# Kernel optimization log

Measured on AMD Instinct MI355X. Metric: run time of the kernel, lower is better.

The kernel has to match this reference:

```python
import jax, jax.numpy as jnp
import numpy as np

L = 4            # num_layers
N_GENES = 2048   # col_dim: rows of x, PPI graph nodes
N_CELLS = 2048   # row_dim: cols of x, KNN graph nodes
E_KNN = 30720    # ~k=15 per cell
E_PPI = 65536    # ~avg degree 32 per gene
NEG_SLOPE = 0.01 # nn.LeakyReLU default


def setup_inputs() -> dict:
    key = jax.random.key(0)
    ks = jax.random.split(key, 9)
    x = jax.random.normal(ks[0], (N_GENES, N_CELLS), jnp.float32)
    knn_edge_index = jax.random.randint(ks[1], (2, E_KNN), 0, N_CELLS)
    ppi_edge_index = jax.random.randint(ks[2], (2, E_PPI), 0, N_GENES)
    s_c = 1.0 / np.sqrt(N_GENES)  # cols side feature dim = col_dim
    s_r = 1.0 / np.sqrt(N_CELLS)  # rows side feature dim = row_dim
    col_Wl = jax.random.normal(ks[3], (L, N_GENES, N_GENES), jnp.float32) * s_c
    col_bl = jnp.zeros((L, N_GENES), jnp.float32)
    col_Wr = jax.random.normal(ks[4], (L, N_GENES, N_GENES), jnp.float32) * s_c
    row_Wl = jax.random.normal(ks[5], (L, N_CELLS, N_CELLS), jnp.float32) * s_r
    row_bl = jnp.zeros((L, N_CELLS), jnp.float32)
    row_Wr = jax.random.normal(ks[6], (L, N_CELLS, N_CELLS), jnp.float32) * s_r
    return dict(x=x, knn_edge_index=knn_edge_index, ppi_edge_index=ppi_edge_index,
                col_Wl=col_Wl, col_bl=col_bl, col_Wr=col_Wr,
                row_Wl=row_Wl, row_bl=row_bl, row_Wr=row_Wr)


def _sage(h, edge_index, Wl, bl, Wr):
    # PyG SAGEConv (mean aggr): out = lin_l(mean_{j->i} h_j) + lin_r(h_i)
    src, tgt = edge_index[0], edge_index[1]
    n = h.shape[0]
    summed = jax.ops.segment_sum(h[src], tgt, num_segments=n)          # [n, d]
    cnt = jax.ops.segment_sum(jnp.ones((src.shape[0],), h.dtype), tgt, num_segments=n)
    mean = summed / jnp.maximum(cnt, 1.0)[:, None]
    return mean @ Wl + bl + h @ Wr


def reference(x, knn_edge_index, ppi_edge_index,
              col_Wl, col_bl, col_Wr, row_Wl, row_bl, row_Wr):
    # Dropout is identity in eval mode; layer = SAGEConv -> LeakyReLU on both sides.
    h = x  # [N_GENES, N_CELLS]
    for i in range(L):
        # cols side: operate on h.T [N_CELLS, N_GENES] over KNN graph
        h = jax.nn.leaky_relu(_sage(h.T, knn_edge_index, col_Wl[i], col_bl[i], col_Wr[i]),
                              negative_slope=NEG_SLOPE).T
        # rows side: operate on h [N_GENES, N_CELLS] over PPI graph
        h = jax.nn.leaky_relu(_sage(h, ppi_edge_index, row_Wl[i], row_bl[i], row_Wr[i]),
                              negative_slope=NEG_SLOPE)
    return h
```

## Files before the change

kernel.cpp:

```cpp
#include <hip/hip_runtime.h>
#include <stdint.h>

#define NSZ 2048
#define NLAYERS 4

typedef __attribute__((ext_vector_type(4))) float f32x4;
typedef __attribute__((ext_vector_type(4))) _Float16 f16x4;
typedef __attribute__((ext_vector_type(8))) _Float16 f16x8;

__device__ __forceinline__ void gload_lds16(const void* g, void* l) {
  __builtin_amdgcn_global_load_lds((const __attribute__((address_space(1))) void*)g,
                                   (__attribute__((address_space(3))) void*)l, 16, 0, 0);
}

__global__ void k_zero(int* __restrict__ p, int n) {
  int i = blockIdx.x * 256 + threadIdx.x;
  if (i < n) p[i] = 0;
}

__global__ void k_count(const int* __restrict__ tgt, int E, int* __restrict__ cnt) {
  int e = blockIdx.x * 256 + threadIdx.x;
  if (e < E) atomicAdd(&cnt[tgt[e] & (NSZ - 1)], 1);
}

__global__ __launch_bounds__(1024) void k_scan(
    const int* __restrict__ cntA, int* __restrict__ offA, int* __restrict__ curA,
    float* __restrict__ invA, int EA,
    const int* __restrict__ cntB, int* __restrict__ offB, int* __restrict__ curB,
    float* __restrict__ invB, int EB) {
  const int* cnt; int* off; int* cur; float* inv; int E;
  if (blockIdx.x == 0) { cnt = cntA; off = offA; cur = curA; inv = invA; E = EA; }
  else                 { cnt = cntB; off = offB; cur = curB; inv = invB; E = EB; }
  __shared__ int sa[2048], sb[2048];
  int t = threadIdx.x;
  sa[t] = cnt[t]; sa[t + 1024] = cnt[t + 1024];
  __syncthreads();
  int* s = sa; int* d = sb;
  for (int dd = 1; dd < 2048; dd <<= 1) {
    for (int i = t; i < 2048; i += 1024)
      d[i] = s[i] + ((i >= dd) ? s[i - dd] : 0);
    __syncthreads();
    int* tmp = s; s = d; d = tmp;
  }
  for (int i = t; i < 2048; i += 1024) {
    int o = (i == 0) ? 0 : s[i - 1];
    off[i] = o; cur[i] = o;
    int c = cnt[i];
    inv[i] = 1.0f / (float)((c > 1) ? c : 1);
  }
  if (t == 0) off[2048] = E;
}

__global__ void k_fill(const int* __restrict__ src, const int* __restrict__ tgt, int E,
                       int* __restrict__ cur, int* __restrict__ srcs) {
  int e = blockIdx.x * 256 + threadIdx.x;
  if (e < E) {
    int p = atomicAdd(&cur[tgt[e] & (NSZ - 1)], 1);
    if (p >= 0 && p < E) srcs[p] = src[e] & (NSZ - 1);
  }
}

__global__ __launch_bounds__(256) void k_transpose_cvt(const float* __restrict__ s,
                                                       _Float16* __restrict__ Ah,
                                                       _Float16* __restrict__ Al) {
  __shared__ float tile[64][65];
  const int tid = threadIdx.x;
  const int r0 = blockIdx.y << 6, c0 = blockIdx.x << 6;
#pragma unroll
  for (int it = 0; it < 4; ++it) {
    int e = it * 256 + tid;
    int r = e >> 4;
    int c = (e & 15) << 2;
    f32x4 v = *(const f32x4*)&s[(size_t)(r0 + r) * NSZ + c0 + c];
#pragma unroll
    for (int j = 0; j < 4; ++j) tile[r][c + j] = v[j];
  }
  __syncthreads();
#pragma unroll
  for (int it = 0; it < 4; ++it) {
    int e = it * 256 + tid;
    int r = e >> 4;
    int c4 = (e & 15) << 2;
    f16x4 hi, lo;
#pragma unroll
    for (int j = 0; j < 4; ++j) {
      float x = tile[c4 + j][r];
      _Float16 h = (_Float16)x;
      hi[j] = h;
      lo[j] = (_Float16)(x - (float)h);
    }
    int m = c0 + r;
    size_t rowb = (size_t)m << 12;
    int byte = ((r0 + c4) << 1) ^ (((m >> 1) & 3) << 4);
    *(f16x4*)((char*)Ah + rowb + byte) = hi;
    *(f16x4*)((char*)Al + rowb + byte) = lo;
  }
}

__global__ __launch_bounds__(256) void k_cvtB(const float* __restrict__ Wl,
                                              const float* __restrict__ Wr,
                                              _Float16* __restrict__ Bh,
                                              _Float16* __restrict__ Bl) {
  __shared__ float tile[64][65];
  const float* W = blockIdx.z ? Wr : Wl;
  const int nbase = blockIdx.z ? NSZ : 0;
  const int tid = threadIdx.x;
  const int k0 = blockIdx.y << 6;
  const int n0 = blockIdx.x << 6;
#pragma unroll
  for (int it = 0; it < 4; ++it) {
    int e = it * 256 + tid;
    int r = e >> 4;
    int c = (e & 15) << 2;
    f32x4 v = *(const f32x4*)&W[(size_t)(k0 + r) * NSZ + n0 + c];
#pragma unroll
    for (int j = 0; j < 4; ++j) tile[r][c + j] = v[j];
  }
  __syncthreads();
#pragma unroll
  for (int it = 0; it < 4; ++it) {
    int e = it * 256 + tid;
    int r = e >> 4;
    int c4 = (e & 15) << 2;
    f16x4 hi, lo;
#pragma unroll
    for (int j = 0; j < 4; ++j) {
      float x = tile[c4 + j][r];
      _Float16 h = (_Float16)x;
      hi[j] = h;
      lo[j] = (_Float16)(x - (float)h);
    }
    int n = nbase + n0 + r;
    size_t rowb = (size_t)n << 12;
    int byte = ((k0 + c4) << 1) ^ (((n >> 1) & 3) << 4);
    *(f16x4*)((char*)Bh + rowb + byte) = hi;
    *(f16x4*)((char*)Bl + rowb + byte) = lo;
  }
}

__global__ __launch_bounds__(256, 2) void k_gemm16(
    const _Float16* __restrict__ Ah, const _Float16* __restrict__ Al,
    const _Float16* __restrict__ Bh, const _Float16* __restrict__ Bl,
    float* __restrict__ C) {
  __shared__ __align__(128) _Float16 lds[2][4][128][32];
  const int tid = threadIdx.x;
  const int w = tid >> 6;
  const int lane = tid & 63;
  int bid = blockIdx.x;
  bid = ((bid & 7) << 6) | (bid >> 3);
  const int bm = bid & 15;
  const int bn = bid >> 4;
  const int m0 = bm << 7;
  const int n0 = bn << 7;
  const int wm = (w & 1) << 6;
  const int wn = (w >> 1) << 6;

  f32x4 acc[4][4];
#pragma unroll
  for (int i = 0; i < 4; ++i)
#pragma unroll
    for (int j = 0; j < 4; ++j)
#pragma unroll
      for (int r = 0; r < 4; ++r) acc[i][j][r] = 0.f;

  const int srow0 = (w << 5) + (lane >> 2);
  const int scol = (lane & 3) << 3;
  const int l15 = lane & 15;
  const int ks16 = (lane >> 4) << 4;

  const size_t aoff = (size_t)(m0 + srow0) * NSZ + scol;
  const size_t boff = (size_t)(n0 + srow0) * NSZ + scol;

#define STAGE(buf, kk)                                                     \
  do {                                                                     \
    _Pragma("unroll") for (int q = 0; q < 2; ++q) {                        \
      const size_t go = (size_t)(q << 4) * NSZ + (kk);                     \
      const int dr = ((w << 1) + q) << 4;                                  \
      gload_lds16(&Ah[aoff + go], &lds[buf][0][dr][0]);                    \
      gload_lds16(&Al[aoff + go], &lds[buf][1][dr][0]);                    \
      gload_lds16(&Bh[boff + go], &lds[buf][2][dr][0]);                    \
      gload_lds16(&Bl[boff + go], &lds[buf][3][dr][0]);                    \
    }                                                                      \
  } while (0)

  STAGE(0, 0);

  int cur = 0;
  for (int k0 = 0; k0 < NSZ; k0 += 32) {
    const int nxt = cur ^ 1;
    if (k0 + 32 < NSZ) {
      STAGE(nxt, k0 + 32);
      asm volatile("s_waitcnt vmcnt(8)" ::: "memory");
    } else {
      asm volatile("s_waitcnt vmcnt(0)" ::: "memory");
    }
    __builtin_amdgcn_s_barrier();
    asm volatile("" ::: "memory");

    f16x8 afh[4], afl[4], bfh[4], bfl[4];
#pragma unroll
    for (int f = 0; f < 4; ++f) {
      const int ra = wm + (f << 4) + l15;
      const int ca = ks16 ^ (((ra >> 1) & 3) << 4);
      afh[f] = *(const f16x8*)((const char*)&lds[cur][0][ra][0] + ca);
      afl[f] = *(const f16x8*)((const char*)&lds[cur][1][ra][0] + ca);
      const int rb = wn + (f << 4) + l15;
      const int cb = ks16 ^ (((rb >> 1) & 3) << 4);
      bfh[f] = *(const f16x8*)((const char*)&lds[cur][2][rb][0] + cb);
      bfl[f] = *(const f16x8*)((const char*)&lds[cur][3][rb][0] + cb);
    }
    __builtin_amdgcn_s_setprio(1);
#pragma unroll
    for (int i = 0; i < 4; ++i)
#pragma unroll
      for (int j = 0; j < 4; ++j) {
        acc[i][j] = __builtin_amdgcn_mfma_f32_16x16x32_f16(afh[i], bfh[j], acc[i][j], 0, 0, 0);
        acc[i][j] = __builtin_amdgcn_mfma_f32_16x16x32_f16(afh[i], bfl[j], acc[i][j], 0, 0, 0);
        acc[i][j] = __builtin_amdgcn_mfma_f32_16x16x32_f16(afl[i], bfh[j], acc[i][j], 0, 0, 0);
      }
    __builtin_amdgcn_s_setprio(0);
    asm volatile("s_waitcnt lgkmcnt(0)" ::: "memory");
    __builtin_amdgcn_s_barrier();
    asm volatile("" ::: "memory");
    cur = nxt;
  }
#undef STAGE

  const int cr = (lane >> 4) << 2;
#pragma unroll
  for (int i = 0; i < 4; ++i)
#pragma unroll
    for (int j = 0; j < 4; ++j) {
      float* Cp = &C[(size_t)(m0 + wm + (i << 4) + cr) * 4096 + n0 + wn + (j << 4) + l15];
#pragma unroll
      for (int r = 0; r < 4; ++r) Cp[(size_t)r * 4096] = acc[i][j][r];
    }
}

__global__ __launch_bounds__(256) void k_fuse(const float* __restrict__ Cb,
                                              const int* __restrict__ off,
                                              const int* __restrict__ srcs,
                                              const float* __restrict__ inv,
                                              const float* __restrict__ bias,
                                              float* __restrict__ outF,
                                              _Float16* __restrict__ oh,
                                              _Float16* __restrict__ ol,
                                              int mode, int E) {
  __shared__ float tile[64][65];
  const int tid = threadIdx.x;
  const int w = tid >> 6;
  const int lane = tid & 63;
  const int lin = blockIdx.x;
  const int xcd = lin & 7;
  const int idx = lin >> 3;
  const int f0 = ((xcd << 2) | (idx & 3)) << 6;
  const int t0 = (idx >> 2) << 6;
  const int fc = f0 + lane;
  const float b = bias[fc];

  for (int it = 0; it < 16; ++it) {
    int lt = (w << 4) + it;
    int c = t0 + lt;
    int e0 = off[c], e1 = off[c + 1];
    if (e1 > E) e1 = E;
    if (e0 < 0) e0 = 0;
    float acc = 0.f;
    int e = e0;
    while (e + 8 <= e1) {
      float p[8];
#pragma unroll
      for (int q = 0; q < 8; ++q)
        p[q] = Cb[(size_t)(srcs[e + q] & (NSZ - 1)) * 4096 + fc];
#pragma unroll
      for (int q = 0; q < 8; ++q) acc += p[q];
      e += 8;
    }
    while (e < e1) { acc += Cb[(size_t)(srcs[e] & (NSZ - 1)) * 4096 + fc]; ++e; }
    float val = acc * inv[c] + Cb[(size_t)c * 4096 + 2048 + fc] + b;
    val = (val > 0.f) ? val : 0.01f * val;
    tile[lt][lane] = val;
  }
  __syncthreads();
  for (int it = 0; it < 4; ++it) {
    int f = it * 256 + tid;
    int r = f >> 4;
    int c4 = (f & 15) << 2;
    if (mode) {
      f16x4 hi, lo;
#pragma unroll
      for (int j = 0; j < 4; ++j) {
        float x = tile[c4 + j][r];
        _Float16 h = (_Float16)x;
        hi[j] = h;
        lo[j] = (_Float16)(x - (float)h);
      }
      int m = f0 + r;
      size_t rowb = (size_t)m << 12;
      int byte = ((t0 + c4) << 1) ^ (((m >> 1) & 3) << 4);
      *(f16x4*)((char*)oh + rowb + byte) = hi;
      *(f16x4*)((char*)ol + rowb + byte) = lo;
    } else {
      f32x4 v;
#pragma unroll
      for (int j = 0; j < 4; ++j) v[j] = tile[r][c4 + j];
      *(f32x4*)&outF[(size_t)(t0 + r) * NSZ + f0 + c4] = v;
    }
  }
}

extern "C" void kernel_launch(void* const* d_in, const int* in_sizes, int n_in,
                              void* d_out, int out_size, void* d_ws, size_t ws_size,
                              hipStream_t stream) {
  (void)n_in; (void)out_size; (void)ws_size;
  const float* x      = (const float*)d_in[0];
  const int*   knn    = (const int*)d_in[1];
  const int*   ppi    = (const int*)d_in[2];
  const float* col_Wl = (const float*)d_in[3];
  const float* col_bl = (const float*)d_in[4];
  const float* col_Wr = (const float*)d_in[5];
  const float* row_Wl = (const float*)d_in[6];
  const float* row_bl = (const float*)d_in[7];
  const float* row_Wr = (const float*)d_in[8];
  float* out = (float*)d_out;
  const int E_knn = in_sizes[1] / 2;
  const int E_ppi = in_sizes[2] / 2;
  const size_t NN = (size_t)NSZ * NSZ;

  char* ws = (char*)d_ws;
  size_t off_b = 0;
  int*   cnt_knn = (int*)(ws + off_b);   off_b += 2048 * 4;
  int*   cnt_ppi = (int*)(ws + off_b);   off_b += 2048 * 4;
  int*   off_knn = (int*)(ws + off_b);   off_b += 2064 * 4;
  int*   off_ppi = (int*)(ws + off_b);   off_b += 2064 * 4;
  int*   cur_knn = (int*)(ws + off_b);   off_b += 2048 * 4;
  int*   cur_ppi = (int*)(ws + off_b);   off_b += 2048 * 4;
  float* inv_knn = (float*)(ws + off_b); off_b += 2048 * 4;
  float* inv_ppi = (float*)(ws + off_b); off_b += 2048 * 4;
  int*   src_knn = (int*)(ws + off_b);   off_b += (size_t)((E_knn + 63) & ~63) * 4;
  int*   src_ppi = (int*)(ws + off_b);   off_b += (size_t)((E_ppi + 63) & ~63) * 4;
  off_b = (off_b + 255) & ~(size_t)255;
  float*     Cbuf = (float*)(ws + off_b);     off_b += NN * 2 * 4;
  _Float16*  Ahw  = (_Float16*)(ws + off_b);  off_b += NN * 2;
  _Float16*  Alw  = (_Float16*)(ws + off_b);  off_b += NN * 2;
  _Float16*  Bhw  = (_Float16*)(ws + off_b);  off_b += NN * 2 * 2;
  _Float16*  Blw  = (_Float16*)(ws + off_b);  off_b += NN * 2 * 2;

  k_zero<<<16, 256, 0, stream>>>(cnt_knn, 4096);
  k_count<<<(E_knn + 255) / 256, 256, 0, stream>>>(knn + E_knn, E_knn, cnt_knn);
  k_count<<<(E_ppi + 255) / 256, 256, 0, stream>>>(ppi + E_ppi, E_ppi, cnt_ppi);
  k_scan<<<2, 1024, 0, stream>>>(cnt_knn, off_knn, cur_knn, inv_knn, E_knn,
                                 cnt_ppi, off_ppi, cur_ppi, inv_ppi, E_ppi);
  k_fill<<<(E_knn + 255) / 256, 256, 0, stream>>>(knn, knn + E_knn, E_knn, cur_knn, src_knn);
  k_fill<<<(E_ppi + 255) / 256, 256, 0, stream>>>(ppi, ppi + E_ppi, E_ppi, cur_ppi, src_ppi);

  {
    dim3 g(32, 32);
    k_transpose_cvt<<<g, 256, 0, stream>>>(x, Ahw, Alw);
  }

  for (int i = 0; i < NLAYERS; ++i) {
    dim3 gb(32, 32, 2);
    k_cvtB<<<gb, 256, 0, stream>>>(col_Wl + (size_t)i * NN, col_Wr + (size_t)i * NN, Bhw, Blw);
    k_gemm16<<<512, 256, 0, stream>>>(Ahw, Alw, Bhw, Blw, Cbuf);
    k_fuse<<<1024, 256, 0, stream>>>(Cbuf, off_knn, src_knn, inv_knn,
                                     col_bl + (size_t)i * NSZ, out, Ahw, Alw, 1, E_knn);
    k_cvtB<<<gb, 256, 0, stream>>>(row_Wl + (size_t)i * NN, row_Wr + (size_t)i * NN, Bhw, Blw);
    k_gemm16<<<512, 256, 0, stream>>>(Ahw, Alw, Bhw, Blw, Cbuf);
    k_fuse<<<1024, 256, 0, stream>>>(Cbuf, off_ppi, src_ppi, inv_ppi,
                                     row_bl + (size_t)i * NSZ, out, Ahw, Alw,
                                     (i < NLAYERS - 1) ? 1 : 0, E_ppi);
  }
}
```

Measured before the change: 1.669 ms.

## Add phase-interleaved pipelined split-fp16 GEMM and nontemporal stores in fuse kernel

Adds k_gemm16p, a GEMM variant that splits each k-step's global-to-LDS prefetch into four parts. Each part is interleaved with LDS fragment reads and one quadrant of the MFMA work, separated by barriers, and the compute phases run at raised wave priority. The goal is to hide global load latency behind matrix work more finely than the original double-buffered loop. It is used only for the cols-side GEMM. The original k_gemm16, still used for the rows side, is reduced to a plain __syncthreads-based loop without the explicit vmcnt wait or priority hints. The fuse kernel's output and f16 hi/lo stores become nontemporal to reduce cache pollution, with the risk that the following GEMM re-reads that data from slower memory.

```diff
diff --git a/kernel.cpp b/kernel.cpp
--- a/kernel.cpp
+++ b/kernel.cpp
@@ -184,18 +184,12 @@
   } while (0)
 
   STAGE(0, 0);
+  __syncthreads();
 
   int cur = 0;
   for (int k0 = 0; k0 < NSZ; k0 += 32) {
     const int nxt = cur ^ 1;
-    if (k0 + 32 < NSZ) {
-      STAGE(nxt, k0 + 32);
-      asm volatile("s_waitcnt vmcnt(8)" ::: "memory");
-    } else {
-      asm volatile("s_waitcnt vmcnt(0)" ::: "memory");
-    }
-    __builtin_amdgcn_s_barrier();
-    asm volatile("" ::: "memory");
+    if (k0 + 32 < NSZ) STAGE(nxt, k0 + 32);
 
     f16x8 afh[4], afl[4], bfh[4], bfl[4];
 #pragma unroll
@@ -209,7 +203,6 @@
       bfh[f] = *(const f16x8*)((const char*)&lds[cur][2][rb][0] + cb);
       bfl[f] = *(const f16x8*)((const char*)&lds[cur][3][rb][0] + cb);
     }
-    __builtin_amdgcn_s_setprio(1);
 #pragma unroll
     for (int i = 0; i < 4; ++i)
 #pragma unroll
@@ -218,13 +211,147 @@
         acc[i][j] = __builtin_amdgcn_mfma_f32_16x16x32_f16(afh[i], bfl[j], acc[i][j], 0, 0, 0);
         acc[i][j] = __builtin_amdgcn_mfma_f32_16x16x32_f16(afl[i], bfh[j], acc[i][j], 0, 0, 0);
       }
+    __syncthreads();
+    cur = nxt;
+  }
+#undef STAGE
+
+  const int cr = (lane >> 4) << 2;
+#pragma unroll
+  for (int i = 0; i < 4; ++i)
+#pragma unroll
+    for (int j = 0; j < 4; ++j) {
+      float* Cp = &C[(size_t)(m0 + wm + (i << 4) + cr) * 4096 + n0 + wn + (j << 4) + l15];
+#pragma unroll
+      for (int r = 0; r < 4; ++r) Cp[(size_t)r * 4096] = acc[i][j][r];
+    }
+}
+
+__global__ __launch_bounds__(256, 2) void k_gemm16p(
+    const _Float16* __restrict__ Ah, const _Float16* __restrict__ Al,
+    const _Float16* __restrict__ Bh, const _Float16* __restrict__ Bl,
+    float* __restrict__ C) {
+  __shared__ __align__(128) _Float16 lds[2][4][128][32];
+  const int tid = threadIdx.x;
+  const int w = tid >> 6;
+  const int lane = tid & 63;
+  int bid = blockIdx.x;
+  bid = ((bid & 7) << 6) | (bid >> 3);
+  const int bm = bid & 15;
+  const int bn = bid >> 4;
+  const int m0 = bm << 7;
+  const int n0 = bn << 7;
+  const int wm = (w & 1) << 6;
+  const int wn = (w >> 1) << 6;
+
+  f32x4 acc[4][4];
+#pragma unroll
+  for (int i = 0; i < 4; ++i)
+#pragma unroll
+    for (int j = 0; j < 4; ++j)
+#pragma unroll
+      for (int r = 0; r < 4; ++r) acc[i][j][r] = 0.f;
+
+  const int srow0 = (w << 5) + (lane >> 2);
+  const int scol = (lane & 3) << 3;
+  const int l15 = lane & 15;
+  const int ks16 = (lane >> 4) << 4;
+
+  const size_t aoff = (size_t)(m0 + srow0) * NSZ + scol;
+  const size_t boff = (size_t)(n0 + srow0) * NSZ + scol;
+
+#define SPART(buf, kk, p)                                                   \
+  do {                                                                      \
+    const int q_ = (p) >> 1;                                                \
+    const size_t go_ = (size_t)(q_ << 4) * NSZ + (size_t)(kk);              \
+    const int dr_ = ((w << 1) + q_) << 4;                                   \
+    if (((p) & 1) == 0) {                                                   \
+      gload_lds16(&Ah[aoff + go_], &lds[buf][0][dr_][0]);                   \
+      gload_lds16(&Al[aoff + go_], &lds[buf][1][dr_][0]);                   \
+    } else {                                                                \
+      gload_lds16(&Bh[boff + go_], &lds[buf][2][dr_][0]);                   \
+      gload_lds16(&Bl[boff + go_], &lds[buf][3][dr_][0]);                   \
+    }                                                                       \
+  } while (0)
+
+#define RDA(f)                                                              \
+  do {                                                                      \
+    const int ra_ = wm + ((f) << 4) + l15;                                  \
+    const int ca_ = ks16 ^ (((ra_ >> 1) & 3) << 4);                         \
+    afh[f] = *(const f16x8*)((const char*)&lds[cur][0][ra_][0] + ca_);      \
+    afl[f] = *(const f16x8*)((const char*)&lds[cur][1][ra_][0] + ca_);      \
+  } while (0)
+
+#define RDB(f)                                                              \
+  do {                                                                      \
+    const int rb_ = wn + ((f) << 4) + l15;                                  \
+    const int cb_ = ks16 ^ (((rb_ >> 1) & 3) << 4);                         \
+    bfh[f] = *(const f16x8*)((const char*)&lds[cur][2][rb_][0] + cb_);      \
+    bfl[f] = *(const f16x8*)((const char*)&lds[cur][3][rb_][0] + cb_);      \
+  } while (0)
+
+#define TRIPLE(i, j)                                                                        \
+  acc[i][j] = __builtin_amdgcn_mfma_f32_16x16x32_f16(afh[i], bfh[j], acc[i][j], 0, 0, 0);   \
+  acc[i][j] = __builtin_amdgcn_mfma_f32_16x16x32_f16(afh[i], bfl[j], acc[i][j], 0, 0, 0);   \
+  acc[i][j] = __builtin_amdgcn_mfma_f32_16x16x32_f16(afl[i], bfh[j], acc[i][j], 0, 0, 0);
+
+#define QUAD(i0, j0)                                                        \
+  TRIPLE(i0, j0) TRIPLE(i0, (j0) + 1) TRIPLE((i0) + 1, j0) TRIPLE((i0) + 1, (j0) + 1)
+
+#define BAR() asm volatile("s_barrier" ::: "memory")
+#define WAITVM0() asm volatile("s_waitcnt vmcnt(0)" ::: "memory")
+
+  SPART(0, 0, 0); SPART(0, 0, 1); SPART(0, 0, 2); SPART(0, 0, 3);
+
+  for (int t = 0; t < 63; ++t) {
+    const int cur = t & 1;
+    const int nxt = cur ^ 1;
+    const int kn = (t + 1) << 5;
+    WAITVM0();
+    BAR();
+    f16x8 afh[4], afl[4], bfh[4], bfl[4];
+    SPART(nxt, kn, 0); SPART(nxt, kn, 1);
+    RDA(0); RDA(1); RDB(0); RDB(1);
+    __builtin_amdgcn_s_setprio(1);
+    QUAD(0, 0)
     __builtin_amdgcn_s_setprio(0);
-    asm volatile("s_waitcnt lgkmcnt(0)" ::: "memory");
-    __builtin_amdgcn_s_barrier();
-    asm volatile("" ::: "memory");
-    cur = nxt;
-  }
-#undef STAGE
+    BAR();
+    SPART(nxt, kn, 2);
+    RDB(2); RDB(3);
+    __builtin_amdgcn_s_setprio(1);
+    QUAD(0, 2)
+    __builtin_amdgcn_s_setprio(0);
+    BAR();
+    SPART(nxt, kn, 3);
+    RDA(2); RDA(3);
+    __builtin_amdgcn_s_setprio(1);
+    QUAD(2, 2)
+    __builtin_amdgcn_s_setprio(0);
+    BAR();
+    __builtin_amdgcn_s_setprio(1);
+    QUAD(2, 0)
+    __builtin_amdgcn_s_setprio(0);
+  }
+  {
+    const int cur = 1;
+    WAITVM0();
+    BAR();
+    f16x8 afh[4], afl[4], bfh[4], bfl[4];
+    RDA(0); RDA(1); RDB(0); RDB(1);
+    QUAD(0, 0)
+    RDB(2); RDB(3);
+    QUAD(0, 2)
+    RDA(2); RDA(3);
+    QUAD(2, 2)
+    QUAD(2, 0)
+  }
+#undef SPART
+#undef RDA
+#undef RDB
+#undef TRIPLE
+#undef QUAD
+#undef BAR
+#undef WAITVM0
 
   const int cr = (lane >> 4) << 2;
 #pragma unroll
@@ -297,13 +424,13 @@
       int m = f0 + r;
       size_t rowb = (size_t)m << 12;
       int byte = ((t0 + c4) << 1) ^ (((m >> 1) & 3) << 4);
-      *(f16x4*)((char*)oh + rowb + byte) = hi;
-      *(f16x4*)((char*)ol + rowb + byte) = lo;
+      __builtin_nontemporal_store(hi, (f16x4*)((char*)oh + rowb + byte));
+      __builtin_nontemporal_store(lo, (f16x4*)((char*)ol + rowb + byte));
     } else {
       f32x4 v;
 #pragma unroll
       for (int j = 0; j < 4; ++j) v[j] = tile[r][c4 + j];
-      *(f32x4*)&outF[(size_t)(t0 + r) * NSZ + f0 + c4] = v;
+      __builtin_nontemporal_store(v, (f32x4*)&outF[(size_t)(t0 + r) * NSZ + f0 + c4]);
     }
   }
 }
@@ -361,7 +488,7 @@
   for (int i = 0; i < NLAYERS; ++i) {
     dim3 gb(32, 32, 2);
     k_cvtB<<<gb, 256, 0, stream>>>(col_Wl + (size_t)i * NN, col_Wr + (size_t)i * NN, Bhw, Blw);
-    k_gemm16<<<512, 256, 0, stream>>>(Ahw, Alw, Bhw, Blw, Cbuf);
+    k_gemm16p<<<512, 256, 0, stream>>>(Ahw, Alw, Bhw, Blw, Cbuf);
     k_fuse<<<1024, 256, 0, stream>>>(Cbuf, off_knn, src_knn, inv_knn,
                                      col_bl + (size_t)i * NSZ, out, Ahw, Alw, 1, E_knn);
     k_cvtB<<<gb, 256, 0, stream>>>(row_Wl + (size_t)i * NN, row_Wr + (size_t)i * NN, Bhw, Blw);
```

New measurement: 1.594 ms. 1.05x faster.

## Load A fragments directly to registers and split GEMM body into interleaved phases

Applied to the files above, without the earlier changes.

The GEMM stops staging A through LDS. Each wave loads its A hi/lo fragments straight from global memory into double-buffered registers, so the A layout no longer needs the XOR swizzle and the producers drop it. Only B stays in LDS, and its prefetch for the next k-step is split into four quarter-phases interleaved with MFMA groups separated by barriers, aiming to overlap loads with compute and halve LDS use. The fuse kernel's gather loop becomes a single predicated, unrolled loop, and the final fp32 output uses nontemporal stores. The risks are uncoalesced direct global loads for A and extra barriers per k-step.

```diff
diff --git a/kernel.cpp b/kernel.cpp
--- a/kernel.cpp
+++ b/kernel.cpp
@@ -91,7 +91,7 @@
     }
     int m = c0 + r;
     size_t rowb = (size_t)m << 12;
-    int byte = ((r0 + c4) << 1) ^ (((m >> 1) & 3) << 4);
+    int byte = (r0 + c4) << 1;
     *(f16x4*)((char*)Ah + rowb + byte) = hi;
     *(f16x4*)((char*)Al + rowb + byte) = lo;
   }
@@ -138,11 +138,11 @@
   }
 }
 
-__global__ __launch_bounds__(256, 2) void k_gemm16(
+__global__ __launch_bounds__(256, 2) void k_gemm16r(
     const _Float16* __restrict__ Ah, const _Float16* __restrict__ Al,
     const _Float16* __restrict__ Bh, const _Float16* __restrict__ Bl,
     float* __restrict__ C) {
-  __shared__ __align__(128) _Float16 lds[2][4][128][32];
+  __shared__ __align__(128) _Float16 lds[2][2][128][32];
   const int tid = threadIdx.x;
   const int w = tid >> 6;
   const int lane = tid & 63;
@@ -167,64 +167,88 @@
   const int scol = (lane & 3) << 3;
   const int l15 = lane & 15;
   const int ks16 = (lane >> 4) << 4;
-
-  const size_t aoff = (size_t)(m0 + srow0) * NSZ + scol;
+  const int khalf = (lane >> 4) << 3;
+
   const size_t boff = (size_t)(n0 + srow0) * NSZ + scol;
 
-#define STAGE(buf, kk)                                                     \
-  do {                                                                     \
-    _Pragma("unroll") for (int q = 0; q < 2; ++q) {                        \
-      const size_t go = (size_t)(q << 4) * NSZ + (kk);                     \
-      const int dr = ((w << 1) + q) << 4;                                  \
-      gload_lds16(&Ah[aoff + go], &lds[buf][0][dr][0]);                    \
-      gload_lds16(&Al[aoff + go], &lds[buf][1][dr][0]);                    \
-      gload_lds16(&Bh[boff + go], &lds[buf][2][dr][0]);                    \
-      gload_lds16(&Bl[boff + go], &lds[buf][3][dr][0]);                    \
-    }                                                                      \
-  } while (0)
-
-  STAGE(0, 0);
-
-  int cur = 0;
-  for (int k0 = 0; k0 < NSZ; k0 += 32) {
-    const int nxt = cur ^ 1;
-    if (k0 + 32 < NSZ) {
-      STAGE(nxt, k0 + 32);
-      asm volatile("s_waitcnt vmcnt(8)" ::: "memory");
-    } else {
-      asm volatile("s_waitcnt vmcnt(0)" ::: "memory");
-    }
-    __builtin_amdgcn_s_barrier();
-    asm volatile("" ::: "memory");
-
-    f16x8 afh[4], afl[4], bfh[4], bfl[4];
-#pragma unroll
-    for (int f = 0; f < 4; ++f) {
-      const int ra = wm + (f << 4) + l15;
-      const int ca = ks16 ^ (((ra >> 1) & 3) << 4);
-      afh[f] = *(const f16x8*)((const char*)&lds[cur][0][ra][0] + ca);
-      afl[f] = *(const f16x8*)((const char*)&lds[cur][1][ra][0] + ca);
-      const int rb = wn + (f << 4) + l15;
-      const int cb = ks16 ^ (((rb >> 1) & 3) << 4);
-      bfh[f] = *(const f16x8*)((const char*)&lds[cur][2][rb][0] + cb);
-      bfl[f] = *(const f16x8*)((const char*)&lds[cur][3][rb][0] + cb);
-    }
-    __builtin_amdgcn_s_setprio(1);
-#pragma unroll
-    for (int i = 0; i < 4; ++i)
-#pragma unroll
-      for (int j = 0; j < 4; ++j) {
-        acc[i][j] = __builtin_amdgcn_mfma_f32_16x16x32_f16(afh[i], bfh[j], acc[i][j], 0, 0, 0);
-        acc[i][j] = __builtin_amdgcn_mfma_f32_16x16x32_f16(afh[i], bfl[j], acc[i][j], 0, 0, 0);
-        acc[i][j] = __builtin_amdgcn_mfma_f32_16x16x32_f16(afl[i], bfh[j], acc[i][j], 0, 0, 0);
-      }
-    __builtin_amdgcn_s_setprio(0);
-    asm volatile("s_waitcnt lgkmcnt(0)" ::: "memory");
-    __builtin_amdgcn_s_barrier();
-    asm volatile("" ::: "memory");
-    cur = nxt;
-  }
-#undef STAGE
+#define AFR(dst, PTR, f, kk)                                                 \
+  dst[f] = *(const f16x8*)((PTR) +                                           \
+      (((size_t)(m0 + wm + ((f) << 4) + l15)) << 11) + (size_t)(kk) + khalf);
+
+#define SPB(buf, kk, q, hl)                                                  \
+  gload_lds16(((hl) ? Bl : Bh) + boff + (size_t)((q) << 4) * NSZ + (size_t)(kk), \
+              &lds[buf][hl][((w << 1) + (q)) << 4][0]);
+
+#define RDB2(CUR, f)                                                         \
+  { const int rb_ = wn + ((f) << 4) + l15;                                   \
+    const int cb_ = ks16 ^ (((rb_ >> 1) & 3) << 4);                          \
+    bfh[f] = *(const f16x8*)((const char*)&lds[CUR][0][rb_][0] + cb_);       \
+    bfl[f] = *(const f16x8*)((const char*)&lds[CUR][1][rb_][0] + cb_); }
+
+#define TR2(AH, AL, i, j)                                                                 \
+  acc[i][j] = __builtin_amdgcn_mfma_f32_16x16x32_f16(AH[i], bfh[j], acc[i][j], 0, 0, 0);  \
+  acc[i][j] = __builtin_amdgcn_mfma_f32_16x16x32_f16(AH[i], bfl[j], acc[i][j], 0, 0, 0);  \
+  acc[i][j] = __builtin_amdgcn_mfma_f32_16x16x32_f16(AL[i], bfh[j], acc[i][j], 0, 0, 0);
+
+#define QU2(AH, AL, i0, j0)                                                  \
+  TR2(AH, AL, i0, j0) TR2(AH, AL, i0, (j0) + 1)                              \
+  TR2(AH, AL, (i0) + 1, j0) TR2(AH, AL, (i0) + 1, (j0) + 1)
+
+#define BODY(CAH, CAL, NAH, NAL, CUR, NXT, T, PRE)                           \
+  {                                                                          \
+    asm volatile("s_waitcnt vmcnt(0)" ::: "memory");                         \
+    asm volatile("s_barrier" ::: "memory");                                  \
+    const int kn_ = ((T) + 1) << 5;                                          \
+    f16x8 bfh[4], bfl[4];                                                    \
+     \
+    if (PRE) { SPB(NXT, kn_, 0, 0)                                           \
+               AFR(NAH, Ah, 0, kn_) AFR(NAL, Al, 0, kn_)                     \
+               AFR(NAH, Ah, 1, kn_) AFR(NAL, Al, 1, kn_) }                   \
+    RDB2(CUR, 0) RDB2(CUR, 1)                                                \
+    __builtin_amdgcn_s_setprio(1);                                           \
+    QU2(CAH, CAL, 0, 0)                                                      \
+    __builtin_amdgcn_s_setprio(0);                                           \
+    asm volatile("s_barrier" ::: "memory");                                  \
+             \
+    if (PRE) { SPB(NXT, kn_, 0, 1)                                           \
+               AFR(NAH, Ah, 2, kn_) AFR(NAL, Al, 2, kn_)                     \
+               AFR(NAH, Ah, 3, kn_) AFR(NAL, Al, 3, kn_) }                   \
+    RDB2(CUR, 2) RDB2(CUR, 3)                                                \
+    __builtin_amdgcn_s_setprio(1);                                           \
+    QU2(CAH, CAL, 0, 2)                                                      \
+    __builtin_amdgcn_s_setprio(0);                                           \
+    asm volatile("s_barrier" ::: "memory");                                  \
+                                             \
+    if (PRE) { SPB(NXT, kn_, 1, 0) }                                         \
+    __builtin_amdgcn_s_setprio(1);                                           \
+    QU2(CAH, CAL, 2, 2)                                                      \
+    __builtin_amdgcn_s_setprio(0);                                           \
+    asm volatile("s_barrier" ::: "memory");                                  \
+                                             \
+    if (PRE) { SPB(NXT, kn_, 1, 1) }                                         \
+    __builtin_amdgcn_s_setprio(1);                                           \
+    QU2(CAH, CAL, 2, 0)                                                      \
+    __builtin_amdgcn_s_setprio(0);                                           \
+  }
+
+  f16x8 ahe[4], ale[4], aho[4], alo[4];
+#pragma unroll
+  for (int f = 0; f < 4; ++f) { AFR(ahe, Ah, f, 0) AFR(ale, Al, f, 0) }
+  SPB(0, 0, 0, 0) SPB(0, 0, 0, 1) SPB(0, 0, 1, 0) SPB(0, 0, 1, 1)
+
+  for (int tt = 0; tt < 31; ++tt) {
+    BODY(ahe, ale, aho, alo, 0, 1, (tt << 1), 1)
+    BODY(aho, alo, ahe, ale, 1, 0, ((tt << 1) | 1), 1)
+  }
+  BODY(ahe, ale, aho, alo, 0, 1, 62, 1)
+  BODY(aho, alo, ahe, ale, 1, 0, 63, 0)
+
+#undef AFR
+#undef SPB
+#undef RDB2
+#undef TR2
+#undef QU2
+#undef BODY
 
   const int cr = (lane >> 4) << 2;
 #pragma unroll
@@ -265,17 +289,19 @@
     if (e1 > E) e1 = E;
     if (e0 < 0) e0 = 0;
     float acc = 0.f;
-    int e = e0;
-    while (e + 8 <= e1) {
-      float p[8];
-#pragma unroll
-      for (int q = 0; q < 8; ++q)
-        p[q] = Cb[(size_t)(srcs[e + q] & (NSZ - 1)) * 4096 + fc];
-#pragma unroll
-      for (int q = 0; q < 8; ++q) acc += p[q];
-      e += 8;
-    }
-    while (e < e1) { acc += Cb[(size_t)(srcs[e] & (NSZ - 1)) * 4096 + fc]; ++e; }
+    if (e0 < e1) {
+      for (int e = e0; e < e1; e += 8) {
+        float p[8];
+#pragma unroll
+        for (int q = 0; q < 8; ++q) {
+          int ee = e + q;
+          int ec = (ee < e1) ? ee : (e1 - 1);
+          p[q] = Cb[(size_t)(srcs[ec] & (NSZ - 1)) * 4096 + fc];
+        }
+#pragma unroll
+        for (int q = 0; q < 8; ++q) acc += ((e + q) < e1) ? p[q] : 0.f;
+      }
+    }
     float val = acc * inv[c] + Cb[(size_t)c * 4096 + 2048 + fc] + b;
     val = (val > 0.f) ? val : 0.01f * val;
     tile[lt][lane] = val;
@@ -296,14 +322,14 @@
       }
       int m = f0 + r;
       size_t rowb = (size_t)m << 12;
-      int byte = ((t0 + c4) << 1) ^ (((m >> 1) & 3) << 4);
+      int byte = (t0 + c4) << 1;
       *(f16x4*)((char*)oh + rowb + byte) = hi;
       *(f16x4*)((char*)ol + rowb + byte) = lo;
     } else {
       f32x4 v;
 #pragma unroll
       for (int j = 0; j < 4; ++j) v[j] = tile[r][c4 + j];
-      *(f32x4*)&outF[(size_t)(t0 + r) * NSZ + f0 + c4] = v;
+      __builtin_nontemporal_store(v, (f32x4*)&outF[(size_t)(t0 + r) * NSZ + f0 + c4]);
     }
   }
 }
@@ -361,11 +387,11 @@
   for (int i = 0; i < NLAYERS; ++i) {
     dim3 gb(32, 32, 2);
     k_cvtB<<<gb, 256, 0, stream>>>(col_Wl + (size_t)i * NN, col_Wr + (size_t)i * NN, Bhw, Blw);
-    k_gemm16<<<512, 256, 0, stream>>>(Ahw, Alw, Bhw, Blw, Cbuf);
+    k_gemm16r<<<512, 256, 0, stream>>>(Ahw, Alw, Bhw, Blw, Cbuf);
     k_fuse<<<1024, 256, 0, stream>>>(Cbuf, off_knn, src_knn, inv_knn,
                                      col_bl + (size_t)i * NSZ, out, Ahw, Alw, 1, E_knn);
     k_cvtB<<<gb, 256, 0, stream>>>(row_Wl + (size_t)i * NN, row_Wr + (size_t)i * NN, Bhw, Blw);
-    k_gemm16<<<512, 256, 0, stream>>>(Ahw, Alw, Bhw, Blw, Cbuf);
+    k_gemm16r<<<512, 256, 0, stream>>>(Ahw, Alw, Bhw, Blw, Cbuf);
     k_fuse<<<1024, 256, 0, stream>>>(Cbuf, off_ppi, src_ppi, inv_ppi,
                                      row_bl + (size_t)i * NSZ, out, Ahw, Alw,
                                      (i < NLAYERS - 1) ? 1 : 0, E_ppi);
```

New measurement: 2.024 ms. +21.3%, slower.
